# Performance work log

Hardware: AMD Instinct MI355X
Metric: run time of the kernel (lower is better)

## Reference

```python
import jax, jax.numpy as jnp
import numpy as np

EMBED = 256
HEADS = 8
HD = EMBED // HEADS
LEVELS = 4
POINTS = 4
FFN_H = 1024
BS = 8
LQ = 900
SHAPES = [(100, 100), (50, 50), (25, 25), (13, 13)]


def setup_inputs() -> dict:
    key = jax.random.key(0)
    ks = jax.random.split(key, 20)
    nv = sum(h * w for h, w in SHAPES)
    starts = np.cumsum([0] + [h * w for h, w in SHAPES])[:-1]
    inp = {
        "queries": jax.random.normal(ks[0], (BS, LQ, EMBED), jnp.float32),
        "memory": jax.random.normal(ks[1], (BS, nv, EMBED), jnp.float32),
        "query_pos": jax.random.normal(ks[2], (BS, LQ, EMBED), jnp.float32),
        "reference_points": jax.random.uniform(ks[3], (BS, LQ, LEVELS, 4), jnp.float32) * 0.9 + 0.05,
        "spatial_shapes": jnp.asarray(SHAPES, jnp.int32),
        "level_start_index": jnp.asarray(starts, jnp.int32),
    }
    def lin(k, din, dout):
        k1, k2 = jax.random.split(k)
        w = jax.random.normal(k1, (din, dout), jnp.float32) * 0.02
        b = jax.random.normal(k2, (dout,), jnp.float32) * 0.01
        return w, b
    specs = [("Wq", "bq", EMBED, EMBED), ("Wk", "bk", EMBED, EMBED), ("Wv", "bv", EMBED, EMBED),
             ("Wo", "bo", EMBED, EMBED), ("Wvd", "bvd", EMBED, EMBED),
             ("Woff", "boff", EMBED, HEADS * LEVELS * POINTS * 2),
             ("Watt", "batt", EMBED, HEADS * LEVELS * POINTS),
             ("Wop", "bop", EMBED, EMBED), ("Wg", "bg", 2 * EMBED, 2 * EMBED),
             ("W1", "b1", EMBED, FFN_H), ("W2", "b2", FFN_H, EMBED)]
    for i, (wn, bn, di, do) in enumerate(specs):
        w, b = lin(ks[4 + i], di, do)
        inp[wn] = w
        inp[bn] = b
    for n in ["ln1", "ln2", "ln3"]:
        inp[n + "_s"] = jnp.ones((EMBED,), jnp.float32)
        inp[n + "_b"] = jnp.zeros((EMBED,), jnp.float32)
    return inp


def _ln(x, s, b):
    m = jnp.mean(x, -1, keepdims=True)
    v = jnp.mean(jnp.square(x - m), -1, keepdims=True)
    return (x - m) * jax.lax.rsqrt(v + 1e-5) * s + b


def _bilinear(v_l, lx, ly, H, W):
    # v_l: [bs,h,H*W,hd]; lx,ly: [bs,h,lq,p] normalized in [0,1]
    # grid_sample(align_corners=False, padding=zeros) semantics
    px = lx * W - 0.5
    py = ly * H - 0.5
    x0 = jnp.floor(px)
    y0 = jnp.floor(py)
    wx = px - x0
    wy = py - y0
    x0i = x0.astype(jnp.int32)
    y0i = y0.astype(jnp.int32)
    bs, h, lq, p = lx.shape
    out = jnp.zeros((bs, h, lq, p, HD), v_l.dtype)
    for dy in (0, 1):
        for dx in (0, 1):
            xi = x0i + dx
            yi = y0i + dy
            w = (wx if dx else 1.0 - wx) * (wy if dy else 1.0 - wy)
            valid = (xi >= 0) & (xi < W) & (yi >= 0) & (yi < H)
            idx = jnp.clip(yi, 0, H - 1) * W + jnp.clip(xi, 0, W - 1)
            g = jnp.take_along_axis(v_l, idx.reshape(bs, h, lq * p)[..., None], axis=2)
            g = g.reshape(bs, h, lq, p, HD)
            out = out + w[..., None] * jnp.where(valid[..., None], g, 0.0)
    return out


def reference(queries, memory, query_pos, reference_points, spatial_shapes, level_start_index,
              Wq, bq, Wk, bk, Wv, bv, Wo, bo, Wvd, bvd, Woff, boff, Watt, batt, Wop, bop,
              Wg, bg, W1, b1, W2, b2, ln1_s, ln1_b, ln2_s, ln2_b, ln3_s, ln3_b):
    bs, lq, _ = queries.shape
    shp = np.asarray(spatial_shapes)
    st = np.asarray(level_start_index)

    # ---- self attention (pre-norm, q=k=x+pos, v=x) ----
    x = _ln(queries, ln1_s, ln1_b)
    qk = x + query_pos
    Q = (qk @ Wq + bq).reshape(bs, lq, HEADS, HD)
    K = (qk @ Wk + bk).reshape(bs, lq, HEADS, HD)
    V = (x @ Wv + bv).reshape(bs, lq, HEADS, HD)
    scores = jnp.einsum('bqhd,bkhd->bhqk', Q, K) * (1.0 / np.sqrt(HD))
    attn = jax.nn.softmax(scores, axis=-1)
    sa = jnp.einsum('bhqk,bkhd->bqhd', attn, V).reshape(bs, lq, EMBED) @ Wo + bo
    x1 = queries + sa  # dropout is identity in eval

    # ---- MS-deformable cross attention ----
    y = _ln(x1, ln2_s, ln2_b)
    qc = y + query_pos
    val = (memory @ Wvd + bvd).reshape(bs, -1, HEADS, HD).transpose(0, 2, 1, 3)  # [bs,h,Nv,hd]
    off = (qc @ Woff + boff).reshape(bs, lq, HEADS, LEVELS, POINTS, 2)
    aw = jax.nn.softmax((qc @ Watt + batt).reshape(bs, lq, HEADS, LEVELS * POINTS), axis=-1)
    aw = aw.reshape(bs, lq, HEADS, LEVELS, POINTS)
    rp = reference_points[:, :, None, :, None, :]  # [bs,lq,1,L,1,4]
    loc = rp[..., :2] + off / POINTS * rp[..., 2:] * 0.5  # [bs,lq,h,L,p,2]

    out = jnp.zeros((bs, HEADS, lq, HD), queries.dtype)
    for l in range(LEVELS):
        H, W = int(shp[l, 0]), int(shp[l, 1])
        s0 = int(st[l])
        v_l = val[:, :, s0:s0 + H * W]
        lx = jnp.transpose(loc[:, :, :, l, :, 0], (0, 2, 1, 3))  # [bs,h,lq,p]
        ly = jnp.transpose(loc[:, :, :, l, :, 1], (0, 2, 1, 3))
        samp = _bilinear(v_l, lx, ly, H, W)  # [bs,h,lq,p,hd]
        w = jnp.transpose(aw[:, :, :, l], (0, 2, 1, 3))  # [bs,h,lq,p]
        out = out + jnp.sum(w[..., None] * samp, axis=3)
    cross = out.transpose(0, 2, 1, 3).reshape(bs, lq, EMBED) @ Wop + bop

    # ---- gated fusion ----
    gi = jnp.concatenate([x1, cross], axis=-1)
    g = jax.nn.sigmoid(gi @ Wg + bg)
    x2 = g[..., :EMBED] * x1 + g[..., EMBED:] * cross

    # ---- FFN ----
    z = _ln(x2, ln3_s, ln3_b)
    ffn = jax.nn.relu(z @ W1 + b1) @ W2 + b2
    return (x2 + ffn, aw, loc)
```

## Files before the change

kernel.cpp:

```cpp
#include <hip/hip_runtime.h>
#include <hip/hip_bf16.h>
#include <math.h>

#define BB 8
#define LQ 900
#define EE 256
#define NH 8
#define HD 32
#define NL 4
#define NP 4
#define FFN_H 1024

typedef __bf16 bf16x8 __attribute__((ext_vector_type(8)));
typedef float f32x4 __attribute__((ext_vector_type(4)));
typedef unsigned short u16x8 __attribute__((ext_vector_type(8)));

__device__ __forceinline__ unsigned short f2b(float f) {
    union { float f; unsigned int u; } v; v.f = f;
    unsigned int u = v.u;
    unsigned int r = (u + 0x7fffu + ((u >> 16) & 1u)) >> 16;
    return (unsigned short)r;
}
__device__ __forceinline__ float b2f(unsigned short h) {
    union { unsigned int u; float f; } v; v.u = ((unsigned int)h) << 16; return v.f;
}

typedef __attribute__((address_space(3))) unsigned int* lds_ptr_t;
typedef const __attribute__((address_space(1))) unsigned int* gbl_ptr_t;
#define GLOAD16(g, l) __builtin_amdgcn_global_load_lds((gbl_ptr_t)(g), (lds_ptr_t)(l), 16, 0, 0)
#define VMCNT(n) asm volatile("s_waitcnt vmcnt(" #n ")" ::: "memory")

struct TDesc { const float* src; unsigned short* dst; int K, N, tile0; };
struct TPack {
    TDesc d[12];
    const float *bq, *bk, *boff, *batt;
    float *bqk, *boa;
    const float *Wop_src, *Wg_src, *bop_src, *bg_src;
    unsigned short* WopRow;
    float* bgg;
};

__global__ __launch_bounds__(256) void prep_kernel(
    TPack p,
    const float* __restrict__ queries, const float* __restrict__ qpos,
    const float* __restrict__ ln1_s, const float* __restrict__ ln1_b,
    unsigned short* __restrict__ x_b, unsigned short* __restrict__ qk_b)
{
    const int bi = blockIdx.x;
    const int t = threadIdx.x;

    if (bi < 1248) {
        int di = 0;
#pragma unroll
        for (int i = 1; i < 12; ++i) if (bi >= p.d[i].tile0) di = i;
        TDesc d = p.d[di];
        int tt = bi - d.tile0;
        int tn = (d.N + 31) >> 5;
        int tk = tt / tn, tc = tt % tn;
        __shared__ float tile[32][33];
        int tx = t & 31, ty = t >> 5;
#pragma unroll
        for (int i = 0; i < 4; ++i) {
            int kk = tk * 32 + ty + i * 8, nn = tc * 32 + tx;
// ... 35 lines not shown
    }
    {
        const int row = bi - 1286;
        const int w = t >> 6, lane = t & 63;
        __shared__ float red[4];
        float v = queries[(size_t)row * EE + t];
        float sum = v;
#pragma unroll
        for (int o = 32; o; o >>= 1) sum += __shfl_xor(sum, o, 64);
        if (lane == 0) red[w] = sum;
        __syncthreads();
        float mean = (red[0] + red[1] + red[2] + red[3]) * (1.0f / 256.0f);
        __syncthreads();
        float dd = v - mean;
        float sq = dd * dd;
#pragma unroll
        for (int o = 32; o; o >>= 1) sq += __shfl_xor(sq, o, 64);
        if (lane == 0) red[w] = sq;
        __syncthreads();
        float var = (red[0] + red[1] + red[2] + red[3]) * (1.0f / 256.0f);
        float y = dd * rsqrtf(var + 1e-5f) * ln1_s[t] + ln1_b[t];
        x_b[(size_t)row * EE + t]  = f2b(y);
        qk_b[(size_t)row * EE + t] = f2b(y + qpos[(size_t)row * EE + t]);
    }
}

struct GD {
    const unsigned short* A;
    const unsigned short* Bt;
    const float* bias;
    const float* resid;
    float* outF;
    unsigned short* outB;
    const float* lnS; const float* lnB; const float* lnAdd;
    unsigned short* lnOut;
    int M, K, N, ntN, tile0, ldOutB, outBoff, act, ldA;
};
struct GB {
    GD d[3]; int nd, tot;
    const float* castSrc; unsigned short* castDst; long castN;
};

template<int BN>
__global__ __launch_bounds__(256, (BN == 128) ? 4 : 2) void gemm_pipe(GB g) {
    __shared__ __align__(16) unsigned short ldsb[2][(64 + BN) * 32];
    __shared__ float lnred[2][64][2];
    const int tid = threadIdx.x;
    const int l = tid & 63, w = tid >> 6;
    const int wr = w >> 1, wc = w & 1;
    constexpr int NJ = BN / 32;

    int t = blockIdx.x;
    if (t >= g.tot) {
        long i = ((long)(t - g.tot) * 256 + tid) * 8;
        long stride = (long)2048 * 256 * 8;
        for (; i < g.castN; i += stride) {
            float4 a = *(const float4*)(g.castSrc + i);
            float4 b = *(const float4*)(g.castSrc + i + 4);
            u16x8 o;
            o[0] = f2b(a.x); o[1] = f2b(a.y); o[2] = f2b(a.z); o[3] = f2b(a.w);
            o[4] = f2b(b.x); o[5] = f2b(b.y); o[6] = f2b(b.z); o[7] = f2b(b.w);
            *(u16x8*)(g.castDst + i) = o;
        }
        return;
    }
    int d = 0;
    while (d + 1 < g.nd && t >= g.d[d + 1].tile0) ++d;

    auto stage = [&](int dd, int tt, int ks, int pp) {
        const GD& D = g.d[dd];
        const int lda = D.ldA ? D.ldA : D.K;
        int local = tt - D.tile0;
        int m0 = (local / D.ntN) * 64;
        int n0 = (local % D.ntN) * BN;
        unsigned short* base = &ldsb[pp][0];
        {
            int row = w * 16 + (l >> 2);
            int rg = m0 + row; int mm = D.M - 1; rg = rg < mm ? rg : mm;
            int schunk = ((l & 3) ^ ((row >> 1) & 3)) << 4;
            GLOAD16((const char*)(D.A + (size_t)rg * lda + (ks << 5)) + schunk,
                    base + (w * 16) * 32);
        }
#pragma unroll
        for (int ib = 0; ib < BN / 64; ++ib) {
            int row = ib * 64 + w * 16 + (l >> 2);
            int rg = n0 + row; int nn = D.N - 1; rg = rg < nn ? rg : nn;
            int schunk = ((l & 3) ^ ((row >> 1) & 3)) << 4;
            GLOAD16((const char*)(D.Bt + (size_t)rg * D.K + (ks << 5)) + schunk,
                    base + 2048 + (ib * 64 + w * 16) * 32);
        }
    };

    stage(d, t, 0, 0);
    int p = 0;

    while (true) {
        const GD D = g.d[d];
        int local = t - D.tile0;
        const int m0 = (local / D.ntN) * 64;
        const int n0 = (local % D.ntN) * BN;
        const int nk = D.K >> 5;

        f32x4 acc[2][NJ];
#pragma unroll
        for (int i = 0; i < 2; ++i)
#pragma unroll
            for (int j = 0; j < NJ; ++j) acc[i][j] = (f32x4){0.f, 0.f, 0.f, 0.f};

        for (int ks = 0; ks < nk; ++ks) {
            int nt = t, nks = ks + 1, ndd = d;
            bool have = true;
            if (nks == nk) {
                nt = t + gridDim.x; nks = 0;
                if (nt >= g.tot) have = false;
                else { while (ndd + 1 < g.nd && nt >= g.d[ndd + 1].tile0) ++ndd; }
            }
            if (have) {
                stage(ndd, nt, nks, p ^ 1);
                if constexpr (BN == 128) { VMCNT(3); } else { VMCNT(5); }
            } else {
                VMCNT(0);
            }
            __builtin_amdgcn_sched_barrier(0);
            __builtin_amdgcn_s_barrier();
            __builtin_amdgcn_sched_barrier(0);
            {
                const char* base = (const char*)&ldsb[p][0];
                const int rch = ((l >> 4) ^ ((l >> 1) & 3)) << 4;
                bf16x8 af[2];
#pragma unroll
                for (int i = 0; i < 2; ++i) {
                    int row = wr * 32 + i * 16 + (l & 15);
                    af[i] = *(const bf16x8*)(base + row * 64 + rch);
                }
#pragma unroll
                for (int j = 0; j < NJ; ++j) {
                    int row = wc * (BN / 2) + j * 16 + (l & 15);
                    bf16x8 bfr = *(const bf16x8*)(base + 4096 + row * 64 + rch);
#pragma unroll
                    for (int i = 0; i < 2; ++i)
                        acc[i][j] = __builtin_amdgcn_mfma_f32_16x16x32_bf16(af[i], bfr, acc[i][j], 0, 0, 0);
                }
            }
            __builtin_amdgcn_sched_barrier(0);
            __builtin_amdgcn_s_barrier();
            __builtin_amdgcn_sched_barrier(0);
            p ^= 1;
        }

#pragma unroll
        for (int i = 0; i < 2; ++i) {
#pragma unroll
            for (int r = 0; r < 4; ++r) {
                int gm = m0 + wr * 32 + i * 16 + ((l >> 4) << 2) + r;
                if (gm >= D.M) continue;
#pragma unroll
                for (int j = 0; j < NJ; ++j) {
                    int gn = n0 + wc * (BN / 2) + j * 16 + (l & 15);
                    if (gn >= D.N) continue;
                    float v = acc[i][j][r];
                    if (D.bias)  v += D.bias[gn];
                    if (D.resid) v += D.resid[(size_t)gm * D.N + gn];
                    if (D.act == 1)      v = fmaxf(v, 0.f);
                    else if (D.act == 2) v = 1.0f / (1.0f + __expf(-v));
                    acc[i][j][r] = v;
                    if (D.outF) D.outF[(size_t)gm * D.N + gn] = v;
                    if (D.outB) D.outB[(size_t)gm * D.ldOutB + D.outBoff + gn] = f2b(v);
                }
            }
        }

        if constexpr (BN == 256) {
            if (D.lnOut) {
#pragma unroll
                for (int i = 0; i < 2; ++i) {
#pragma unroll
                    for (int r = 0; r < 4; ++r) {
                        float s1 = 0.f, s2 = 0.f;
#pragma unroll
                        for (int j = 0; j < NJ; ++j) {
                            float v = acc[i][j][r];
                            s1 += v; s2 += v * v;
                        }
#pragma unroll
                        for (int o = 1; o <= 8; o <<= 1) {
                            s1 += __shfl_xor(s1, o, 64);
                            s2 += __shfl_xor(s2, o, 64);
                        }
                        if ((l & 15) == 0) {
                            int row = wr * 32 + i * 16 + ((l >> 4) << 2) + r;
                            lnred[wc][row][0] = s1;
                            lnred[wc][row][1] = s2;
                        }
                    }
                }
                __syncthreads();
#pragma unroll
                for (int i = 0; i < 2; ++i) {
#pragma unroll
                    for (int r = 0; r < 4; ++r) {
                        int row = wr * 32 + i * 16 + ((l >> 4) << 2) + r;
                        int gm = m0 + row;
                        if (gm >= D.M) continue;
                        float mean = (lnred[0][row][0] + lnred[1][row][0]) * (1.0f / 256.0f);
                        float msq  = (lnred[0][row][1] + lnred[1][row][1]) * (1.0f / 256.0f);
                        float rs = rsqrtf(msq - mean * mean + 1e-5f);
#pragma unroll
                        for (int j = 0; j < NJ; ++j) {
                            int gn = wc * 128 + j * 16 + (l & 15);
                            float y = (acc[i][j][r] - mean) * rs * D.lnS[gn] + D.lnB[gn]
                                      + D.lnAdd[(size_t)gm * 256 + gn];
                            D.lnOut[(size_t)gm * 256 + gn] = f2b(y);
                        }
                    }
                }
            }
        }

        t += gridDim.x;
        if (t >= g.tot) break;
        while (d + 1 < g.nd && t >= g.d[d + 1].tile0) ++d;
    }
}

#define VGRID 1536

__global__ __launch_bounds__(256) void attn_val(
    const unsigned short* __restrict__ QK, const unsigned short* __restrict__ Vb,
    unsigned short* __restrict__ outB,
    const unsigned short* __restrict__ vA, const unsigned short* __restrict__ vBt,
    const float* __restrict__ vbias, unsigned short* __restrict__ vout,
    int Mv, int vtiles)
{
    __shared__ __align__(16) unsigned short smem[(64 + 128) * 32 * 2];
    const int bid = blockIdx.x;
    const int tid = threadIdx.x;
    const int l = tid & 63, w = tid >> 6;

    if (bid >= 960) {
        const int wr = w >> 1, wc = w & 1;
        int t = bid - 960;
        if (t >= vtiles) return;

        auto stage = [&](int tt, int ks, int pp) {
            unsigned short* base = &smem[pp * 192 * 32];
            int m0 = (tt >> 1) * 64;
            int n0 = (tt & 1) * 128;
            {
                int row = w * 16 + (l >> 2);
                int rg = m0 + row; int mm = Mv - 1; rg = rg < mm ? rg : mm;
                int schunk = ((l & 3) ^ ((row >> 1) & 3)) << 4;
                GLOAD16((const char*)(vA + (size_t)rg * 256 + (ks << 5)) + schunk,
                        base + (w * 16) * 32);
            }
#pragma unroll
            for (int ib = 0; ib < 2; ++ib) {
                int row = ib * 64 + w * 16 + (l >> 2);
                int rg = n0 + row;
                int schunk = ((l & 3) ^ ((row >> 1) & 3)) << 4;
                GLOAD16((const char*)(vBt + (size_t)rg * 256 + (ks << 5)) + schunk,
                        base + 2048 + (ib * 64 + w * 16) * 32);
            }
        };

        stage(t, 0, 0);
        int p = 0;
        while (true) {
            const int m0 = (t >> 1) * 64;
            const int n0 = (t & 1) * 128;

            f32x4 acc[2][4];
#pragma unroll
            for (int i = 0; i < 2; ++i)
#pragma unroll
                for (int j = 0; j < 4; ++j) acc[i][j] = (f32x4){0.f, 0.f, 0.f, 0.f};

            for (int ks = 0; ks < 8; ++ks) {
                int nt = t, nks = ks + 1;
                bool have = true;
                if (nks == 8) {
                    nt = t + VGRID; nks = 0;
                    if (nt >= vtiles) have = false;
                }
                if (have) { stage(nt, nks, p ^ 1); VMCNT(3); }
                else      { VMCNT(0); }
                __builtin_amdgcn_sched_barrier(0);
                __builtin_amdgcn_s_barrier();
                __builtin_amdgcn_sched_barrier(0);
                {
                    const char* base = (const char*)&smem[p * 192 * 32];
                    const int rch = ((l >> 4) ^ ((l >> 1) & 3)) << 4;
                    bf16x8 af[2];
#pragma unroll
                    for (int i = 0; i < 2; ++i) {
                        int row = wr * 32 + i * 16 + (l & 15);
                        af[i] = *(const bf16x8*)(base + row * 64 + rch);
                    }
#pragma unroll
                    for (int j = 0; j < 4; ++j) {
                        int row = wc * 64 + j * 16 + (l & 15);
                        bf16x8 bfr = *(const bf16x8*)(base + 4096 + row * 64 + rch);
#pragma unroll
                        for (int i = 0; i < 2; ++i)
                            acc[i][j] = __builtin_amdgcn_mfma_f32_16x16x32_bf16(af[i], bfr, acc[i][j], 0, 0, 0);
                    }
                }
                __builtin_amdgcn_sched_barrier(0);
                __builtin_amdgcn_s_barrier();
                __builtin_amdgcn_sched_barrier(0);
                p ^= 1;
            }

#pragma unroll
            for (int i = 0; i < 2; ++i) {
#pragma unroll
                for (int r = 0; r < 4; ++r) {
                    int gm = m0 + wr * 32 + i * 16 + ((l >> 4) << 2) + r;
                    if (gm >= Mv) continue;
#pragma unroll
                    for (int j = 0; j < 4; ++j) {
                        int gn = n0 + wc * 64 + j * 16 + (l & 15);
                        float v = acc[i][j][r] + vbias[gn];
                        vout[(size_t)gm * 256 + gn] = f2b(v);
                    }
                }
            }

            t += VGRID;
            if (t >= vtiles) break;
        }
        return;
    }

    const int qt = bid % 15;
    const int bh = bid / 15;
    const int b = bh >> 3, h = bh & 7;

    unsigned short* Ks = smem;
    unsigned short* VT = smem + 2048;
    unsigned short* Ps = smem + 4096;

    const int qrow_w = qt * 64 + w * 16;
// ... 79 lines not shown

#pragma unroll
        for (int s = 0; s < 2; ++s) {
            union { unsigned short u[8]; bf16x8 v; } pb;
#pragma unroll
            for (int j = 0; j < 8; ++j)
                pb.u[j] = pw[(s * 32 + (l >> 4) * 8 + j) * 20 + (l & 15)];
#pragma unroll
            for (int m2 = 0; m2 < 2; ++m2) {
                int dd = m2 * 16 + (l & 15);
                int swz = (((dd & 7) ^ (dd >> 3)) << 4);
                bf16x8 vf = *(const bf16x8*)((const char*)VT + dd * 128 +
                            ((s * 64 + (l >> 4) * 16) ^ swz));
                if (m2 == 0) acc0 = __builtin_amdgcn_mfma_f32_16x16x32_bf16(vf, pb.v, acc0, 0, 0, 0);
                else         acc1 = __builtin_amdgcn_mfma_f32_16x16x32_bf16(vf, pb.v, acc1, 0, 0, 0);
            }
        }
        if (kt < 14) { kvc = kvn; vvc = vvn; }
    }

    float inv = 1.0f / l_run;
    int q = qrow_w + (l & 15);
    if (q < LQ) {
        size_t obase = ((size_t)(b * LQ + q)) * 256 + h * 32;
#pragma unroll
        for (int r = 0; r < 4; ++r) {
            int d0 = (l >> 4) * 4 + r;
            outB[obase + d0]      = f2b(acc0[r] * inv);
            outB[obase + 16 + d0] = f2b(acc1[r] * inv);
        }
    }
}

__global__ __launch_bounds__(256) void sample_fused(
    const float* __restrict__ off_att, const float* __restrict__ refp,
    const unsigned short* __restrict__ val,
    const int* __restrict__ shapes, const int* __restrict__ starts,
    float* __restrict__ aw_out, float* __restrict__ loc_out,
    unsigned short* __restrict__ xs, int NV)
{
    const int row = blockIdx.x;
    const int b = row / LQ;
    const int t = threadIdx.x;
    const int h = t >> 5, d = t & 31;

    __shared__ float l_logit[128];
    __shared__ float l_aw[128];
    __shared__ float l_loc[256];
    __shared__ int l_sh[NL * 2];
    __shared__ int l_st[NL];

    if (t < 128) l_logit[t] = off_att[(size_t)row * 384 + 256 + t];
    {
        float o = off_att[(size_t)row * 384 + t];
        int c = t & 1;
        int lv = (t >> 3) & 3;
        float rc = refp[((size_t)row * 4 + lv) * 4 + c];
        float rs = refp[((size_t)row * 4 + lv) * 4 + 2 + c];
        float loc = rc + o * 0.125f * rs;
        l_loc[t] = loc;
        loc_out[(size_t)row * 256 + t] = loc;
    }
    if (t < NL * 2) l_sh[t] = shapes[t];
    if (t < NL) l_st[t] = starts[t];
    __syncthreads();
    if (t < 128) {
        int hh = t >> 4;
        float mx = -1e30f;
#pragma unroll
        for (int i = 0; i < 16; ++i) mx = fmaxf(mx, l_logit[hh * 16 + i]);
        float sum = 0.f;
#pragma unroll
        for (int i = 0; i < 16; ++i) sum += __expf(l_logit[hh * 16 + i] - mx);
        float aw = __expf(l_logit[t] - mx) / sum;
        l_aw[t] = aw;
        aw_out[(size_t)row * 128 + t] = aw;
    }
    __syncthreads();

    float acc = 0.f;
    const unsigned short* vb = val + (size_t)b * NV * EE + h * HD + d;

#pragma unroll
    for (int lv = 0; lv < NL; ++lv) {
        const int Hh = l_sh[lv * 2], Ww = l_sh[lv * 2 + 1];
        const int s0 = l_st[lv];
#pragma unroll
        for (int p = 0; p < NP; ++p) {
            const int base = ((h * NL + lv) * NP + p) * 2;
            float lx = l_loc[base], ly = l_loc[base + 1];
            float wgt0 = l_aw[h * 16 + lv * NP + p];
            float px = lx * (float)Ww - 0.5f;
            float py = ly * (float)Hh - 0.5f;
            float x0f = floorf(px), y0f = floorf(py);
            float wx = px - x0f, wy = py - y0f;
            int x0 = (int)x0f, y0 = (int)y0f;
#pragma unroll
            for (int dy = 0; dy < 2; ++dy) {
                int yi = y0 + dy;
                bool vy = (yi >= 0) && (yi < Hh);
                int yc = min(max(yi, 0), Hh - 1);
                float wyv = dy ? wy : 1.f - wy;
#pragma unroll
                for (int dx = 0; dx < 2; ++dx) {
                    int xi = x0 + dx;
                    bool vv = vy && (xi >= 0) && (xi < Ww);
                    int xc = min(max(xi, 0), Ww - 1);
                    float wgt = wgt0 * wyv * (dx ? wx : 1.f - wx);
                    float gv = b2f(vb[(size_t)(s0 + yc * Ww + xc) * EE]);
                    acc += vv ? wgt * gv : 0.f;
                }
            }
        }
    }
    xs[(size_t)row * 512 + 256 + t] = f2b(acc);
}

__global__ __launch_bounds__(256) void gate_ln3(
    const float* __restrict__ g, const float* __restrict__ x1,
    const float* __restrict__ cross, const float* __restrict__ s,
    const float* __restrict__ bln, float* __restrict__ x2out,
    unsigned short* __restrict__ zb)
{
    const int row = blockIdx.x;
    const int t = threadIdx.x;
    const int w = t >> 6;
    const int lane = t & 63;
    __shared__ float red[4];

    float g1 = g[(size_t)row * 512 + t];
    float g2 = g[(size_t)row * 512 + 256 + t];
    float v = g1 * x1[(size_t)row * EE + t] + g2 * cross[(size_t)row * EE + t];
    x2out[(size_t)row * EE + t] = v;

    float sum = v;
#pragma unroll
    for (int o = 32; o; o >>= 1) sum += __shfl_xor(sum, o, 64);
    if (lane == 0) red[w] = sum;
    __syncthreads();
    float mean = (red[0] + red[1] + red[2] + red[3]) * (1.0f / 256.0f);
    __syncthreads();

    float d = v - mean;
    float sq = d * d;
#pragma unroll
    for (int o = 32; o; o >>= 1) sq += __shfl_xor(sq, o, 64);
    if (lane == 0) red[w] = sq;
    __syncthreads();
    float var = (red[0] + red[1] + red[2] + red[3]) * (1.0f / 256.0f);

    float y = d * rsqrtf(var + 1e-5f) * s[t] + bln[t];
    zb[(size_t)row * EE + t] = f2b(y);
}

extern "C" void kernel_launch(void* const* d_in, const int* in_sizes, int n_in,
                              void* d_out, int out_size, void* d_ws, size_t ws_size,
                              hipStream_t stream)
{
    const float* queries   = (const float*)d_in[0];
    const float* memory    = (const float*)d_in[1];
    const float* query_pos = (const float*)d_in[2];
    const float* refp      = (const float*)d_in[3];
    const int*   shapes    = (const int*)d_in[4];
    const int*   starts    = (const int*)d_in[5];
    const float* Wq  = (const float*)d_in[6],  *bq  = (const float*)d_in[7];
    const float* Wk  = (const float*)d_in[8],  *bk  = (const float*)d_in[9];
    const float* Wv  = (const float*)d_in[10], *bv  = (const float*)d_in[11];
    const float* Wo  = (const float*)d_in[12], *bo  = (const float*)d_in[13];
    const float* Wvd = (const float*)d_in[14], *bvd = (const float*)d_in[15];
    const float* Woff= (const float*)d_in[16], *boff= (const float*)d_in[17];
    const float* Watt= (const float*)d_in[18], *batt= (const float*)d_in[19];
    const float* Wop = (const float*)d_in[20], *bop = (const float*)d_in[21];
    const float* Wg  = (const float*)d_in[22], *bg  = (const float*)d_in[23];
    const float* W1  = (const float*)d_in[24], *b1  = (const float*)d_in[25];
    const float* W2  = (const float*)d_in[26], *b2  = (const float*)d_in[27];
    const float* ln1_s = (const float*)d_in[28], *ln1_b = (const float*)d_in[29];
    const float* ln2_s = (const float*)d_in[30], *ln2_b = (const float*)d_in[31];
    const float* ln3_s = (const float*)d_in[32], *ln3_b = (const float*)d_in[33];

    const int NV = in_sizes[1] / (BB * EE);
    const int Mq = BB * LQ;
    const int Mv = BB * NV;
    const long memN = (long)Mv * EE;

    char* W8 = (char*)d_ws;
// ... 33 lines not shown
    unsigned short* hidden_b = (unsigned short*)((char*)z_b + (size_t)Mq * 256 * 2);

    float* out0    = (float*)d_out;
    float* aw_out  = out0 + (size_t)Mq * 256;
    float* loc_out = aw_out + (size_t)Mq * 128;

    dim3 blk(256);
    const int tMq = (Mq + 63) / 64;
    const int tv  = (Mv + 63) / 64;

    TPack tp;
    tp.d[0]  = { Wq,             WtQK,             256, 256,    0 };
    tp.d[1]  = { Wk,             WtQK + 256 * 256, 256, 256,   64 };
    tp.d[2]  = { Wv,             WtV,              256, 256,  128 };
    tp.d[3]  = { Wo,             WtO,              256, 256,  192 };
    tp.d[4]  = { Wvd,            WtVD,             256, 256,  256 };
    tp.d[5]  = { Woff,           WtOA,             256, 256,  320 };
    tp.d[6]  = { Watt,           WtOA + 256 * 256, 256, 128,  384 };
    tp.d[7]  = { Wop,            WtOP,             256, 256,  416 };
    tp.d[8]  = { Wg,             WtGF,             512, 512,  480 };
    tp.d[9]  = { Wg + 256 * 512, Wg2T,             256, 512,  608 };
    tp.d[10] = { W1,             Wt1,              256, 1024, 736 };
    tp.d[11] = { W2,             Wt2,             1024, 256,  992 };
    tp.bq = bq; tp.bk = bk; tp.boff = boff; tp.batt = batt;
    tp.bqk = bqk; tp.boa = boa;
    tp.Wop_src = Wop; tp.Wg_src = Wg; tp.bop_src = bop; tp.bg_src = bg;
    tp.WopRow = WopRow; tp.bgg = bgg;
    prep_kernel<<<8486, blk, 0, stream>>>(
        tp, queries, query_pos, ln1_s, ln1_b, x_b, qk_b);

    {
        GB g; g.nd = 3;
        g.d[0] = { qk_b, WtQK, bqk, nullptr, nullptr, qkb,
                   nullptr, nullptr, nullptr, nullptr,
                   Mq, 256, 512, 4, 0, 512, 0, 0, 0 };
        g.d[1] = { x_b, WtV, bv, nullptr, nullptr, vb_buf,
                   nullptr, nullptr, nullptr, nullptr,
                   Mq, 256, 256, 2, tMq * 4, 256, 0, 0, 0 };
        g.d[2] = { Wg2T, WopRow, nullptr, nullptr, nullptr, WtGF,
                   nullptr, nullptr, nullptr, nullptr,
                   512, 256, 256, 2, tMq * 6, 512, 256, 0, 0 };
        g.tot = tMq * 6 + 16;
        g.castSrc = memory; g.castDst = mem_b; g.castN = memN;
        gemm_pipe<128><<<g.tot + 2048, blk, 0, stream>>>(g);
    }

    attn_val<<<960 + VGRID, blk, 0, stream>>>(
        qkb, vb_buf, av_buf, mem_b, WtVD, bvd, val_b, Mv, tv * 2);

    {
        GB g; g.nd = 1;
        g.d[0] = { av_buf, WtO, bo, queries, x1, xs_cat,
                   ln2_s, ln2_b, query_pos, qc_b,
                   Mq, 256, 256, 1, 0, 512, 0, 0, 0 };
        g.tot = tMq;
        g.castSrc = nullptr; g.castDst = nullptr; g.castN = 0;
        gemm_pipe<256><<<tMq, blk, 0, stream>>>(g);
    }

    {
        GB g; g.nd = 1;
        g.d[0] = { qc_b, WtOA, boa, nullptr, off_att, nullptr,
                   nullptr, nullptr, nullptr, nullptr,
                   Mq, 256, 384, 3, 0, 384, 0, 0, 0 };
        g.tot = tMq * 3;
        g.castSrc = nullptr; g.castDst = nullptr; g.castN = 0;
        gemm_pipe<128><<<g.tot, blk, 0, stream>>>(g);
    }

    sample_fused<<<Mq, blk, 0, stream>>>(off_att, refp, val_b, shapes, starts,
                                         aw_out, loc_out, xs_cat, NV);

    {
        GB g; g.nd = 2;
        g.d[0] = { xs_cat + 256, WtOP, bop, nullptr, cross, nullptr,
                   nullptr, nullptr, nullptr, nullptr,
                   Mq, 256, 256, 2, 0, 0, 0, 0, 512 };
        g.d[1] = { xs_cat, WtGF, bgg, nullptr, gbuf, nullptr,
                   nullptr, nullptr, nullptr, nullptr,
                   Mq, 512, 512, 4, tMq * 2, 0, 0, 2, 0 };
        g.tot = tMq * 6;
        g.castSrc = nullptr; g.castDst = nullptr; g.castN = 0;
        gemm_pipe<128><<<g.tot, blk, 0, stream>>>(g);
    }

    gate_ln3<<<Mq, blk, 0, stream>>>(gbuf, x1, cross, ln3_s, ln3_b, x2, z_b);

    {
        GB g; g.nd = 1;
        g.d[0] = { z_b, Wt1, b1, nullptr, nullptr, hidden_b,
                   nullptr, nullptr, nullptr, nullptr,
                   Mq, 256, 1024, 8, 0, 1024, 0, 1, 0 };
        g.tot = tMq * 8;
        g.castSrc = nullptr; g.castDst = nullptr; g.castN = 0;
        gemm_pipe<128><<<g.tot, blk, 0, stream>>>(g);
    }

    {
        GB g; g.nd = 1;
        g.d[0] = { hidden_b, Wt2, b2, x2, out0, nullptr,
                   nullptr, nullptr, nullptr, nullptr,
                   Mq, 1024, 256, 2, 0, 256, 0, 0, 0 };
        g.tot = tMq * 2;
        g.castSrc = nullptr; g.castDst = nullptr; g.castN = 0;
        gemm_pipe<128><<<g.tot, blk, 0, stream>>>(g);
    }
}
```

Baseline: 305.6 us.

## Merge post-attention stages into one cooperative persistent megakernel with grid syncs

Replaces the separate launches after attn_val (output projection, LN2, offset/attention GEMM, sampling, cross/gate GEMMs, gate+LN3, FFN GEMMs) with a single cooperative kernel that runs each stage as a grid-stride loop and separates stages with grid-wide syncs. It also drops the BN=256 GEMM variant with its fused LN epilogue, computing LN2 as a separate row pass inside the megakernel. The aim is to remove launch overhead and inter-kernel gaps. In exchange, each stage loses its own tuned grid and occupancy, tile GEMMs no longer prefetch across tiles, and grid.sync adds its own cost.

After: 657.8 us. 2.15x slower.

```diff
diff --git a/kernel.cpp b/kernel.cpp
--- a/kernel.cpp
+++ b/kernel.cpp
@@ -1,6 +1,9 @@
 #include <hip/hip_runtime.h>
 #include <hip/hip_bf16.h>
+#include <hip/hip_cooperative_groups.h>
 #include <math.h>
+
+namespace cg = cooperative_groups;
 
 #define BB 8
 #define LQ 900
@@ -29,6 +32,7 @@
 typedef const __attribute__((address_space(1))) unsigned int* gbl_ptr_t;
 #define GLOAD16(g, l) __builtin_amdgcn_global_load_lds((gbl_ptr_t)(g), (lds_ptr_t)(l), 16, 0, 0)
 #define VMCNT(n) asm volatile("s_waitcnt vmcnt(" #n ")" ::: "memory")
+#define SBAR() do { __builtin_amdgcn_sched_barrier(0); __builtin_amdgcn_s_barrier(); __builtin_amdgcn_sched_barrier(0); } while (0)
 
 struct TDesc { const float* src; unsigned short* dst; int K, N, tile0; };
 struct TPack {
@@ -130,8 +134,6 @@
     const float* resid;
     float* outF;
     unsigned short* outB;
-    const float* lnS; const float* lnB; const float* lnAdd;
-    unsigned short* lnOut;
     int M, K, N, ntN, tile0, ldOutB, outBoff, act, ldA;
 };
 struct GB {
@@ -139,14 +141,11 @@
     const float* castSrc; unsigned short* castDst; long castN;
 };
 
-template<int BN>
-__global__ __launch_bounds__(256, (BN == 128) ? 4 : 2) void gemm_pipe(GB g) {
-    __shared__ __align__(16) unsigned short ldsb[2][(64 + BN) * 32];
-    __shared__ float lnred[2][64][2];
+__global__ __launch_bounds__(256, 4) void gemm_pipe(GB g) {
+    __shared__ __align__(16) unsigned short ldsb[2][192 * 32];
     const int tid = threadIdx.x;
     const int l = tid & 63, w = tid >> 6;
     const int wr = w >> 1, wc = w & 1;
-    constexpr int NJ = BN / 32;
 
     int t = blockIdx.x;
     if (t >= g.tot) {
@@ -170,21 +169,21 @@
         const int lda = D.ldA ? D.ldA : D.K;
         int local = tt - D.tile0;
         int m0 = (local / D.ntN) * 64;
-        int n0 = (local % D.ntN) * BN;
+        int n0 = (local % D.ntN) * 128;
         unsigned short* base = &ldsb[pp][0];
         {
             int row = w * 16 + (l >> 2);
             int rg = m0 + row; int mm = D.M - 1; rg = rg < mm ? rg : mm;
-            int schunk = ((l & 3) ^ ((row >> 1) & 3)) << 4;
-            GLOAD16((const char*)(D.A + (size_t)rg * lda + (ks << 5)) + schunk,
+            int sch = ((l & 3) ^ ((row >> 1) & 3)) << 4;
+            GLOAD16((const char*)(D.A + (size_t)rg * lda + (ks << 5)) + sch,
                     base + (w * 16) * 32);
         }
 #pragma unroll
-        for (int ib = 0; ib < BN / 64; ++ib) {
+        for (int ib = 0; ib < 2; ++ib) {
             int row = ib * 64 + w * 16 + (l >> 2);
             int rg = n0 + row; int nn = D.N - 1; rg = rg < nn ? rg : nn;
-            int schunk = ((l & 3) ^ ((row >> 1) & 3)) << 4;
-            GLOAD16((const char*)(D.Bt + (size_t)rg * D.K + (ks << 5)) + schunk,
+            int sch = ((l & 3) ^ ((row >> 1) & 3)) << 4;
+            GLOAD16((const char*)(D.Bt + (size_t)rg * D.K + (ks << 5)) + sch,
                     base + 2048 + (ib * 64 + w * 16) * 32);
         }
     };
@@ -196,14 +195,14 @@
         const GD D = g.d[d];
         int local = t - D.tile0;
         const int m0 = (local / D.ntN) * 64;
-        const int n0 = (local % D.ntN) * BN;
+        const int n0 = (local % D.ntN) * 128;
         const int nk = D.K >> 5;
 
-        f32x4 acc[2][NJ];
+        f32x4 acc[2][4];
 #pragma unroll
         for (int i = 0; i < 2; ++i)
 #pragma unroll
-            for (int j = 0; j < NJ; ++j) acc[i][j] = (f32x4){0.f, 0.f, 0.f, 0.f};
+            for (int j = 0; j < 4; ++j) acc[i][j] = (f32x4){0.f, 0.f, 0.f, 0.f};
 
         for (int ks = 0; ks < nk; ++ks) {
             int nt = t, nks = ks + 1, ndd = d;
@@ -213,15 +212,9 @@
                 if (nt >= g.tot) have = false;
                 else { while (ndd + 1 < g.nd && nt >= g.d[ndd + 1].tile0) ++ndd; }
             }
-            if (have) {
-                stage(ndd, nt, nks, p ^ 1);
-                if constexpr (BN == 128) { VMCNT(3); } else { VMCNT(5); }
-            } else {
-                VMCNT(0);
-            }
-            __builtin_amdgcn_sched_barrier(0);
-            __builtin_amdgcn_s_barrier();
-            __builtin_amdgcn_sched_barrier(0);
+            if (have) { stage(ndd, nt, nks, p ^ 1); VMCNT(3); }
+            else      { VMCNT(0); }
+            SBAR();
             {
                 const char* base = (const char*)&ldsb[p][0];
                 const int rch = ((l >> 4) ^ ((l >> 1) & 3)) << 4;
@@ -232,17 +225,15 @@
                     af[i] = *(const bf16x8*)(base + row * 64 + rch);
                 }
 #pragma unroll
-                for (int j = 0; j < NJ; ++j) {
-                    int row = wc * (BN / 2) + j * 16 + (l & 15);
+                for (int j = 0; j < 4; ++j) {
+                    int row = wc * 64 + j * 16 + (l & 15);
                     bf16x8 bfr = *(const bf16x8*)(base + 4096 + row * 64 + rch);
 #pragma unroll
                     for (int i = 0; i < 2; ++i)
                         acc[i][j] = __builtin_amdgcn_mfma_f32_16x16x32_bf16(af[i], bfr, acc[i][j], 0, 0, 0);
                 }
             }
-            __builtin_amdgcn_sched_barrier(0);
-            __builtin_amdgcn_s_barrier();
-            __builtin_amdgcn_sched_barrier(0);
+            SBAR();
             p ^= 1;
         }
 
@@ -253,64 +244,16 @@
                 int gm = m0 + wr * 32 + i * 16 + ((l >> 4) << 2) + r;
                 if (gm >= D.M) continue;
 #pragma unroll
-                for (int j = 0; j < NJ; ++j) {
-                    int gn = n0 + wc * (BN / 2) + j * 16 + (l & 15);
+                for (int j = 0; j < 4; ++j) {
+                    int gn = n0 + wc * 64 + j * 16 + (l & 15);
                     if (gn >= D.N) continue;
                     float v = acc[i][j][r];
                     if (D.bias)  v += D.bias[gn];
                     if (D.resid) v += D.resid[(size_t)gm * D.N + gn];
                     if (D.act == 1)      v = fmaxf(v, 0.f);
                     else if (D.act == 2) v = 1.0f / (1.0f + __expf(-v));
-                    acc[i][j][r] = v;
                     if (D.outF) D.outF[(size_t)gm * D.N + gn] = v;
                     if (D.outB) D.outB[(size_t)gm * D.ldOutB + D.outBoff + gn] = f2b(v);
-                }
-            }
-        }
-
-        if constexpr (BN == 256) {
-            if (D.lnOut) {
-#pragma unroll
-                for (int i = 0; i < 2; ++i) {
-#pragma unroll
-                    for (int r = 0; r < 4; ++r) {
-                        float s1 = 0.f, s2 = 0.f;
-#pragma unroll
-                        for (int j = 0; j < NJ; ++j) {
-                            float v = acc[i][j][r];
-                            s1 += v; s2 += v * v;
-                        }
-#pragma unroll
-                        for (int o = 1; o <= 8; o <<= 1) {
-                            s1 += __shfl_xor(s1, o, 64);
-                            s2 += __shfl_xor(s2, o, 64);
-                        }
-                        if ((l & 15) == 0) {
-                            int row = wr * 32 + i * 16 + ((l >> 4) << 2) + r;
-                            lnred[wc][row][0] = s1;
-                            lnred[wc][row][1] = s2;
-                        }
-                    }
-                }
-                __syncthreads();
-#pragma unroll
-                for (int i = 0; i < 2; ++i) {
-#pragma unroll
-                    for (int r = 0; r < 4; ++r) {
-                        int row = wr * 32 + i * 16 + ((l >> 4) << 2) + r;
-                        int gm = m0 + row;
-                        if (gm >= D.M) continue;
-                        float mean = (lnred[0][row][0] + lnred[1][row][0]) * (1.0f / 256.0f);
-                        float msq  = (lnred[0][row][1] + lnred[1][row][1]) * (1.0f / 256.0f);
-                        float rs = rsqrtf(msq - mean * mean + 1e-5f);
-#pragma unroll
-                        for (int j = 0; j < NJ; ++j) {
-                            int gn = wc * 128 + j * 16 + (l & 15);
-                            float y = (acc[i][j][r] - mean) * rs * D.lnS[gn] + D.lnB[gn]
-                                      + D.lnAdd[(size_t)gm * 256 + gn];
-                            D.lnOut[(size_t)gm * 256 + gn] = f2b(y);
-                        }
-                    }
                 }
             }
         }
@@ -330,7 +273,7 @@
     const float* __restrict__ vbias, unsigned short* __restrict__ vout,
     int Mv, int vtiles)
 {
-    __shared__ __align__(16) unsigned short smem[(64 + 128) * 32 * 2];
+    __shared__ __align__(16) unsigned short smem[192 * 32 * 2];
     const int bid = blockIdx.x;
     const int tid = threadIdx.x;
     const int l = tid & 63, w = tid >> 6;
@@ -347,16 +290,16 @@
             {
                 int row = w * 16 + (l >> 2);
                 int rg = m0 + row; int mm = Mv - 1; rg = rg < mm ? rg : mm;
-                int schunk = ((l & 3) ^ ((row >> 1) & 3)) << 4;
-                GLOAD16((const char*)(vA + (size_t)rg * 256 + (ks << 5)) + schunk,
+                int sch = ((l & 3) ^ ((row >> 1) & 3)) << 4;
+                GLOAD16((const char*)(vA + (size_t)rg * 256 + (ks << 5)) + sch,
                         base + (w * 16) * 32);
             }
 #pragma unroll
             for (int ib = 0; ib < 2; ++ib) {
                 int row = ib * 64 + w * 16 + (l >> 2);
                 int rg = n0 + row;
-                int schunk = ((l & 3) ^ ((row >> 1) & 3)) << 4;
-                GLOAD16((const char*)(vBt + (size_t)rg * 256 + (ks << 5)) + schunk,
+                int sch = ((l & 3) ^ ((row >> 1) & 3)) << 4;
+                GLOAD16((const char*)(vBt + (size_t)rg * 256 + (ks << 5)) + sch,
                         base + 2048 + (ib * 64 + w * 16) * 32);
             }
         };
@@ -382,9 +325,7 @@
                 }
                 if (have) { stage(nt, nks, p ^ 1); VMCNT(3); }
                 else      { VMCNT(0); }
-                __builtin_amdgcn_sched_barrier(0);
-                __builtin_amdgcn_s_barrier();
-                __builtin_amdgcn_sched_barrier(0);
+                SBAR();
                 {
                     const char* base = (const char*)&smem[p * 192 * 32];
                     const int rch = ((l >> 4) ^ ((l >> 1) & 3)) << 4;
@@ -403,9 +344,7 @@
                             acc[i][j] = __builtin_amdgcn_mfma_f32_16x16x32_bf16(af[i], bfr, acc[i][j], 0, 0, 0);
                     }
                 }
-                __builtin_amdgcn_sched_barrier(0);
-                __builtin_amdgcn_s_barrier();
-                __builtin_amdgcn_sched_barrier(0);
+                SBAR();
                 p ^= 1;
             }
 
@@ -551,125 +490,275 @@
     }
 }
 
-__global__ __launch_bounds__(256) void sample_fused(
-    const float* __restrict__ off_att, const float* __restrict__ refp,
-    const unsigned short* __restrict__ val,
-    const int* __restrict__ shapes, const int* __restrict__ starts,
-    float* __restrict__ aw_out, float* __restrict__ loc_out,
-    unsigned short* __restrict__ xs, int NV)
+struct MegaArgs {
+    const unsigned short *av_buf, *WtO;
+    const float *bo, *queries, *qpos, *ln2_s, *ln2_b;
+    float* x1;
+    unsigned short *xs_cat, *qc_b;
+    const unsigned short* WtOA;
+    const float* boa;
+    float* off_att;
+    const float* refp;
+    const unsigned short* val_b;
+    const int *shapes, *starts;
+    float *aw_out, *loc_out;
+    const unsigned short *WtOP, *WtGF;
+    const float *bop, *bgg;
+    float *crossF, *gbuf;
+    const float *ln3_s, *ln3_b;
+    float* x2;
+    unsigned short* z_b;
+    const unsigned short *Wt1, *Wt2;
+    const float *b1, *b2;
+    unsigned short* hidden_b;
+    float* out0;
+    int NV;
+};
+
+__device__ __forceinline__ void tile_gemm(
+    unsigned short* arena,
+    const unsigned short* A, int lda, const unsigned short* Bt,
+    const float* bias, const float* resid,
+    float* outF, unsigned short* outB, int ldOutB, int outBoff,
+    int M, int K, int N, int ntN, int act,
+    int tiles, int bid, int G, int tid)
 {
-    const int row = blockIdx.x;
-    const int b = row / LQ;
-    const int t = threadIdx.x;
-    const int h = t >> 5, d = t & 31;
-
-    __shared__ float l_logit[128];
-    __shared__ float l_aw[128];
-    __shared__ float l_loc[256];
-    __shared__ int l_sh[NL * 2];
-    __shared__ int l_st[NL];
-
-    if (t < 128) l_logit[t] = off_att[(size_t)row * 384 + 256 + t];
+    const int l = tid & 63, w = tid >> 6;
+    const int wr = w >> 1, wc = w & 1;
+    const int nk = K >> 5;
+    for (int t = bid; t < tiles; t += G) {
+        const int m0 = (t / ntN) * 64;
+        const int n0 = (t % ntN) * 128;
+        auto stage = [&](int ks, int pp) {
+            unsigned short* base = arena + pp * 192 * 32;
+            {
+                int row = w * 16 + (l >> 2);
+                int rg = m0 + row; int mm = M - 1; rg = rg < mm ? rg : mm;
+                int sch = ((l & 3) ^ ((row >> 1) & 3)) << 4;
+                GLOAD16((const char*)(A + (size_t)rg * lda + (ks << 5)) + sch,
+                        base + (w * 16) * 32);
+            }
+#pragma unroll
+            for (int ib = 0; ib < 2; ++ib) {
+                int row = ib * 64 + w * 16 + (l >> 2);
+                int rg = n0 + row; int nn = N - 1; rg = rg < nn ? rg : nn;
+                int sch = ((l & 3) ^ ((row >> 1) & 3)) << 4;
+                GLOAD16((const char*)(Bt + (size_t)rg * K + (ks << 5)) + sch,
+                        base + 2048 + (ib * 64 + w * 16) * 32);
+            }
+        };
+        f32x4 acc[2][4];
+#pragma unroll
+        for (int i = 0; i < 2; ++i)
+#pragma unroll
+            for (int j = 0; j < 4; ++j) acc[i][j] = (f32x4){0.f, 0.f, 0.f, 0.f};
+
+        stage(0, 0);
+        int p = 0;
+        for (int ks = 0; ks < nk; ++ks) {
+            if (ks + 1 < nk) { stage(ks + 1, p ^ 1); VMCNT(3); }
+            else             { VMCNT(0); }
+            SBAR();
+            {
+                const char* base = (const char*)(arena + p * 192 * 32);
+                const int rch = ((l >> 4) ^ ((l >> 1) & 3)) << 4;
+                bf16x8 af[2];
+#pragma unroll
+                for (int i = 0; i < 2; ++i) {
+                    int row = wr * 32 + i * 16 + (l & 15);
+                    af[i] = *(const bf16x8*)(base + row * 64 + rch);
+                }
+#pragma unroll
+                for (int j = 0; j < 4; ++j) {
+                    int row = wc * 64 + j * 16 + (l & 15);
+                    bf16x8 bfr = *(const bf16x8*)(base + 4096 + row * 64 + rch);
+#pragma unroll
+                    for (int i = 0; i < 2; ++i)
+                        acc[i][j] = __builtin_amdgcn_mfma_f32_16x16x32_bf16(af[i], bfr, acc[i][j], 0, 0, 0);
+                }
+            }
+            SBAR();
+            p ^= 1;
+        }
+
+#pragma unroll
+        for (int i = 0; i < 2; ++i) {
+#pragma unroll
+            for (int r = 0; r < 4; ++r) {
+                int gm = m0 + wr * 32 + i * 16 + ((l >> 4) << 2) + r;
+                if (gm >= M) continue;
+#pragma unroll
+                for (int j = 0; j < 4; ++j) {
+                    int gn = n0 + wc * 64 + j * 16 + (l & 15);
+                    if (gn >= N) continue;
+                    float v = acc[i][j][r];
+                    if (bias)  v += bias[gn];
+                    if (resid) v += resid[(size_t)gm * N + gn];
+                    if (act == 1)      v = fmaxf(v, 0.f);
+                    else if (act == 2) v = 1.0f / (1.0f + __expf(-v));
+                    if (outF) outF[(size_t)gm * N + gn] = v;
+                    if (outB) outB[(size_t)gm * ldOutB + outBoff + gn] = f2b(v);
+                }
+            }
+        }
+        __syncthreads();
+    }
+}
+
+__global__ __launch_bounds__(256) void mega_kernel(MegaArgs a) {
+    cg::grid_group gg = cg::this_grid();
+    __shared__ __align__(16) unsigned short arena[192 * 32 * 2];
+    const int tid = threadIdx.x;
+    const int bid = blockIdx.x;
+    const int G = gridDim.x;
+    const int w = tid >> 6, lane = tid & 63;
+    float* red = (float*)arena;
+
+    tile_gemm(arena, a.av_buf, 256, a.WtO, a.bo, a.queries, a.x1, a.xs_cat,
+              512, 0, 7200, 256, 256, 2, 0, 226, bid, G, tid);
+    gg.sync();
+
+    for (int row = bid; row < 7200; row += G) {
+        float v = a.x1[(size_t)row * 256 + tid];
+        float sum = v;
+#pragma unroll
+        for (int o = 32; o; o >>= 1) sum += __shfl_xor(sum, o, 64);
+        if (lane == 0) red[w] = sum;
+        __syncthreads();
+        float mean = (red[0] + red[1] + red[2] + red[3]) * (1.0f / 256.0f);
+        __syncthreads();
+        float dd = v - mean;
+        float sq = dd * dd;
+#pragma unroll
+        for (int o = 32; o; o >>= 1) sq += __shfl_xor(sq, o, 64);
+        if (lane == 0) red[w] = sq;
+        __syncthreads();
+        float var = (red[0] + red[1] + red[2] + red[3]) * (1.0f / 256.0f);
+        float y = dd * rsqrtf(var + 1e-5f) * a.ln2_s[tid] + a.ln2_b[tid]
+                  + a.qpos[(size_t)row * 256 + tid];
+        a.qc_b[(size_t)row * 256 + tid] = f2b(y);
+        __syncthreads();
+    }
+    gg.sync();
+
+    tile_gemm(arena, a.qc_b, 256, a.WtOA, a.boa, nullptr, a.off_att, nullptr,
+              0, 0, 7200, 256, 384, 3, 0, 339, bid, G, tid);
+    gg.sync();
+
     {
-        float o = off_att[(size_t)row * 384 + t];
-        int c = t & 1;
-        int lv = (t >> 3) & 3;
-        float rc = refp[((size_t)row * 4 + lv) * 4 + c];
-        float rs = refp[((size_t)row * 4 + lv) * 4 + 2 + c];
-        float loc = rc + o * 0.125f * rs;
-        l_loc[t] = loc;
-        loc_out[(size_t)row * 256 + t] = loc;
-    }
-    if (t < NL * 2) l_sh[t] = shapes[t];
-    if (t < NL) l_st[t] = starts[t];
-    __syncthreads();
-    if (t < 128) {
-        int hh = t >> 4;
-        float mx = -1e30f;
-#pragma unroll
-        for (int i = 0; i < 16; ++i) mx = fmaxf(mx, l_logit[hh * 16 + i]);
-        float sum = 0.f;
-#pragma unroll
-        for (int i = 0; i < 16; ++i) sum += __expf(l_logit[hh * 16 + i] - mx);
-        float aw = __expf(l_logit[t] - mx) / sum;
-        l_aw[t] = aw;
-        aw_out[(size_t)row * 128 + t] = aw;
-    }
-    __syncthreads();
-
-    float acc = 0.f;
-    const unsigned short* vb = val + (size_t)b * NV * EE + h * HD + d;
-
-#pragma unroll
-    for (int lv = 0; lv < NL; ++lv) {
-        const int Hh = l_sh[lv * 2], Ww = l_sh[lv * 2 + 1];
-        const int s0 = l_st[lv];
-#pragma unroll
-        for (int p = 0; p < NP; ++p) {
-            const int base = ((h * NL + lv) * NP + p) * 2;
-            float lx = l_loc[base], ly = l_loc[base + 1];
-            float wgt0 = l_aw[h * 16 + lv * NP + p];
-            float px = lx * (float)Ww - 0.5f;
-            float py = ly * (float)Hh - 0.5f;
-            float x0f = floorf(px), y0f = floorf(py);
-            float wx = px - x0f, wy = py - y0f;
-            int x0 = (int)x0f, y0 = (int)y0f;
-#pragma unroll
-            for (int dy = 0; dy < 2; ++dy) {
-                int yi = y0 + dy;
-                bool vy = (yi >= 0) && (yi < Hh);
-                int yc = min(max(yi, 0), Hh - 1);
-                float wyv = dy ? wy : 1.f - wy;
-#pragma unroll
-                for (int dx = 0; dx < 2; ++dx) {
-                    int xi = x0 + dx;
-                    bool vv = vy && (xi >= 0) && (xi < Ww);
-                    int xc = min(max(xi, 0), Ww - 1);
-                    float wgt = wgt0 * wyv * (dx ? wx : 1.f - wx);
-                    float gv = b2f(vb[(size_t)(s0 + yc * Ww + xc) * EE]);
-                    acc += vv ? wgt * gv : 0.f;
-                }
-            }
-        }
-    }
-    xs[(size_t)row * 512 + 256 + t] = f2b(acc);
-}
-
-__global__ __launch_bounds__(256) void gate_ln3(
-    const float* __restrict__ g, const float* __restrict__ x1,
-    const float* __restrict__ cross, const float* __restrict__ s,
-    const float* __restrict__ bln, float* __restrict__ x2out,
-    unsigned short* __restrict__ zb)
-{
-    const int row = blockIdx.x;
-    const int t = threadIdx.x;
-    const int w = t >> 6;
-    const int lane = t & 63;
-    __shared__ float red[4];
-
-    float g1 = g[(size_t)row * 512 + t];
-    float g2 = g[(size_t)row * 512 + 256 + t];
-    float v = g1 * x1[(size_t)row * EE + t] + g2 * cross[(size_t)row * EE + t];
-    x2out[(size_t)row * EE + t] = v;
-
-    float sum = v;
-#pragma unroll
-    for (int o = 32; o; o >>= 1) sum += __shfl_xor(sum, o, 64);
-    if (lane == 0) red[w] = sum;
-    __syncthreads();
-    float mean = (red[0] + red[1] + red[2] + red[3]) * (1.0f / 256.0f);
-    __syncthreads();
-
-    float d = v - mean;
-    float sq = d * d;
-#pragma unroll
-    for (int o = 32; o; o >>= 1) sq += __shfl_xor(sq, o, 64);
-    if (lane == 0) red[w] = sq;
-    __syncthreads();
-    float var = (red[0] + red[1] + red[2] + red[3]) * (1.0f / 256.0f);
-
-    float y = d * rsqrtf(var + 1e-5f) * s[t] + bln[t];
-    zb[(size_t)row * EE + t] = f2b(y);
+        float* l_logit = (float*)arena;
+        float* l_aw    = l_logit + 128;
+        float* l_loc   = l_aw + 128;
+        int*   l_sh    = (int*)(l_loc + 256);
+        int*   l_st    = l_sh + 8;
+        const int h = tid >> 5, d = tid & 31;
+        for (int row = bid; row < 7200; row += G) {
+            const int b = row / LQ;
+            if (tid < 128) l_logit[tid] = a.off_att[(size_t)row * 384 + 256 + tid];
+            {
+                float o = a.off_att[(size_t)row * 384 + tid];
+                int c = tid & 1;
+                int lv = (tid >> 3) & 3;
+                float rc = a.refp[((size_t)row * 4 + lv) * 4 + c];
+                float rs = a.refp[((size_t)row * 4 + lv) * 4 + 2 + c];
+                float loc = rc + o * 0.125f * rs;
+                l_loc[tid] = loc;
+                a.loc_out[(size_t)row * 256 + tid] = loc;
+            }
+            if (tid < NL * 2) l_sh[tid] = a.shapes[tid];
+            if (tid < NL) l_st[tid] = a.starts[tid];
+            __syncthreads();
+            if (tid < 128) {
+                int hh = tid >> 4;
+                float mx = -1e30f;
+#pragma unroll
+                for (int i = 0; i < 16; ++i) mx = fmaxf(mx, l_logit[hh * 16 + i]);
+                float sum = 0.f;
+#pragma unroll
+                for (int i = 0; i < 16; ++i) sum += __expf(l_logit[hh * 16 + i] - mx);
+                float aw = __expf(l_logit[tid] - mx) / sum;
+                l_aw[tid] = aw;
+                a.aw_out[(size_t)row * 128 + tid] = aw;
+            }
+            __syncthreads();
+
+            float acc = 0.f;
+            const unsigned short* vb = a.val_b + (size_t)b * a.NV * EE + h * HD + d;
+#pragma unroll
+            for (int lv = 0; lv < NL; ++lv) {
+                const int Hh = l_sh[lv * 2], Ww = l_sh[lv * 2 + 1];
+                const int s0 = l_st[lv];
+#pragma unroll
+                for (int p = 0; p < NP; ++p) {
+                    const int base = ((h * NL + lv) * NP + p) * 2;
+                    float lx = l_loc[base], ly = l_loc[base + 1];
+                    float wgt0 = l_aw[h * 16 + lv * NP + p];
+                    float px = lx * (float)Ww - 0.5f;
+                    float py = ly * (float)Hh - 0.5f;
+                    float x0f = floorf(px), y0f = floorf(py);
+                    float wx = px - x0f, wy = py - y0f;
+                    int x0 = (int)x0f, y0 = (int)y0f;
+#pragma unroll
+                    for (int dy = 0; dy < 2; ++dy) {
+                        int yi = y0 + dy;
+                        bool vy = (yi >= 0) && (yi < Hh);
+                        int yc = min(max(yi, 0), Hh - 1);
+                        float wyv = dy ? wy : 1.f - wy;
+#pragma unroll
+                        for (int dx = 0; dx < 2; ++dx) {
+                            int xi = x0 + dx;
+                            bool vv = vy && (xi >= 0) && (xi < Ww);
+                            int xc = min(max(xi, 0), Ww - 1);
+                            float wgt = wgt0 * wyv * (dx ? wx : 1.f - wx);
+                            float gv = b2f(vb[(size_t)(s0 + yc * Ww + xc) * EE]);
+                            acc += vv ? wgt * gv : 0.f;
+                        }
+                    }
+                }
+            }
+            a.xs_cat[(size_t)row * 512 + 256 + tid] = f2b(acc);
+            __syncthreads();
+        }
+    }
+    gg.sync();
+
+    tile_gemm(arena, a.xs_cat + 256, 512, a.WtOP, a.bop, nullptr, a.crossF, nullptr,
+              0, 0, 7200, 256, 256, 2, 0, 226, bid, G, tid);
+    tile_gemm(arena, a.xs_cat, 512, a.WtGF, a.bgg, nullptr, a.gbuf, nullptr,
+              0, 0, 7200, 512, 512, 4, 2, 452, bid, G, tid);
+    gg.sync();
+
+    for (int row = bid; row < 7200; row += G) {
+        float g1 = a.gbuf[(size_t)row * 512 + tid];
+        float g2 = a.gbuf[(size_t)row * 512 + 256 + tid];
+        float v = g1 * a.x1[(size_t)row * 256 + tid] + g2 * a.crossF[(size_t)row * 256 + tid];
+        a.x2[(size_t)row * 256 + tid] = v;
+        float sum = v;
+#pragma unroll
+        for (int o = 32; o; o >>= 1) sum += __shfl_xor(sum, o, 64);
+        if (lane == 0) red[w] = sum;
+        __syncthreads();
+        float mean = (red[0] + red[1] + red[2] + red[3]) * (1.0f / 256.0f);
+        __syncthreads();
+        float dd = v - mean;
+        float sq = dd * dd;
+#pragma unroll
+        for (int o = 32; o; o >>= 1) sq += __shfl_xor(sq, o, 64);
+        if (lane == 0) red[w] = sq;
+        __syncthreads();
+        float var = (red[0] + red[1] + red[2] + red[3]) * (1.0f / 256.0f);
+        float y = dd * rsqrtf(var + 1e-5f) * a.ln3_s[tid] + a.ln3_b[tid];
+        a.z_b[(size_t)row * 256 + tid] = f2b(y);
+        __syncthreads();
+    }
+    gg.sync();
+
+    tile_gemm(arena, a.z_b, 256, a.Wt1, a.b1, nullptr, nullptr, a.hidden_b,
+              1024, 0, 7200, 256, 1024, 8, 1, 904, bid, G, tid);
+    gg.sync();
+
+    tile_gemm(arena, a.hidden_b, 1024, a.Wt2, a.b2, a.x2, a.out0, nullptr,
+              0, 0, 7200, 1024, 256, 2, 0, 226, bid, G, tid);
 }
 
 extern "C" void kernel_launch(void* const* d_in, const int* in_sizes, int n_in,
@@ -769,77 +858,40 @@
     {
         GB g; g.nd = 3;
         g.d[0] = { qk_b, WtQK, bqk, nullptr, nullptr, qkb,
-                   nullptr, nullptr, nullptr, nullptr,
                    Mq, 256, 512, 4, 0, 512, 0, 0, 0 };
         g.d[1] = { x_b, WtV, bv, nullptr, nullptr, vb_buf,
-                   nullptr, nullptr, nullptr, nullptr,
                    Mq, 256, 256, 2, tMq * 4, 256, 0, 0, 0 };
         g.d[2] = { Wg2T, WopRow, nullptr, nullptr, nullptr, WtGF,
-                   nullptr, nullptr, nullptr, nullptr,
                    512, 256, 256, 2, tMq * 6, 512, 256, 0, 0 };
         g.tot = tMq * 6 + 16;
         g.castSrc = memory; g.castDst = mem_b; g.castN = memN;
-        gemm_pipe<128><<<g.tot + 2048, blk, 0, stream>>>(g);
+        gemm_pipe<<<g.tot + 2048, blk, 0, stream>>>(g);
     }
 
     attn_val<<<960 + VGRID, blk, 0, stream>>>(
         qkb, vb_buf, av_buf, mem_b, WtVD, bvd, val_b, Mv, tv * 2);
 
     {
-        GB g; g.nd = 1;
-        g.d[0] = { av_buf, WtO, bo, queries, x1, xs_cat,
-                   ln2_s, ln2_b, query_pos, qc_b,
-                   Mq, 256, 256, 1, 0, 512, 0, 0, 0 };
-        g.tot = tMq;
-        g.castSrc = nullptr; g.castDst = nullptr; g.castN = 0;
-        gemm_pipe<256><<<tMq, blk, 0, stream>>>(g);
-    }
-
-    {
-        GB g; g.nd = 1;
-        g.d[0] = { qc_b, WtOA, boa, nullptr, off_att, nullptr,
-                   nullptr, nullptr, nullptr, nullptr,
-                   Mq, 256, 384, 3, 0, 384, 0, 0, 0 };
-        g.tot = tMq * 3;
-        g.castSrc = nullptr; g.castDst = nullptr; g.castN = 0;
-        gemm_pipe<128><<<g.tot, blk, 0, stream>>>(g);
-    }
-
-    sample_fused<<<Mq, blk, 0, stream>>>(off_att, refp, val_b, shapes, starts,
-                                         aw_out, loc_out, xs_cat, NV);
-
-    {
-        GB g; g.nd = 2;
-        g.d[0] = { xs_cat + 256, WtOP, bop, nullptr, cross, nullptr,
-                   nullptr, nullptr, nullptr, nullptr,
-                   Mq, 256, 256, 2, 0, 0, 0, 0, 512 };
-        g.d[1] = { xs_cat, WtGF, bgg, nullptr, gbuf, nullptr,
-                   nullptr, nullptr, nullptr, nullptr,
-                   Mq, 512, 512, 4, tMq * 2, 0, 0, 2, 0 };
-        g.tot = tMq * 6;
-        g.castSrc = nullptr; g.castDst = nullptr; g.castN = 0;
-        gemm_pipe<128><<<g.tot, blk, 0, stream>>>(g);
-    }
-
-    gate_ln3<<<Mq, blk, 0, stream>>>(gbuf, x1, cross, ln3_s, ln3_b, x2, z_b);
-
-    {
-        GB g; g.nd = 1;
-        g.d[0] = { z_b, Wt1, b1, nullptr, nullptr, hidden_b,
-                   nullptr, nullptr, nullptr, nullptr,
-                   Mq, 256, 1024, 8, 0, 1024, 0, 1, 0 };
-        g.tot = tMq * 8;
-        g.castSrc = nullptr; g.castDst = nullptr; g.castN = 0;
-        gemm_pipe<128><<<g.tot, blk, 0, stream>>>(g);
-    }
-
-    {
-        GB g; g.nd = 1;
-        g.d[0] = { hidden_b, Wt2, b2, x2, out0, nullptr,
-                   nullptr, nullptr, nullptr, nullptr,
-                   Mq, 1024, 256, 2, 0, 256, 0, 0, 0 };
-        g.tot = tMq * 2;
-        g.castSrc = nullptr; g.castDst = nullptr; g.castN = 0;
-        gemm_pipe<128><<<g.tot, blk, 0, stream>>>(g);
+        MegaArgs ma;
+        ma.av_buf = av_buf; ma.WtO = WtO; ma.bo = bo; ma.queries = queries;
+        ma.qpos = query_pos; ma.ln2_s = ln2_s; ma.ln2_b = ln2_b;
+        ma.x1 = x1; ma.xs_cat = xs_cat; ma.qc_b = qc_b;
+        ma.WtOA = WtOA; ma.boa = boa; ma.off_att = off_att;
+        ma.refp = refp; ma.val_b = val_b; ma.shapes = shapes; ma.starts = starts;
+        ma.aw_out = aw_out; ma.loc_out = loc_out;
+        ma.WtOP = WtOP; ma.WtGF = WtGF; ma.bop = bop; ma.bgg = bgg;
+        ma.crossF = cross; ma.gbuf = gbuf;
+        ma.ln3_s = ln3_s; ma.ln3_b = ln3_b; ma.x2 = x2; ma.z_b = z_b;
+        ma.Wt1 = Wt1; ma.Wt2 = Wt2; ma.b1 = b1; ma.b2 = b2;
+        ma.hidden_b = hidden_b; ma.out0 = out0;
+        ma.NV = NV;
+
+        int nb = 0;
+        hipOccupancyMaxActiveBlocksPerMultiprocessor(&nb, (const void*)mega_kernel, 256, 0);
+        if (nb < 1) nb = 1;
+        int G = nb * 256;
+        if (G > 1536) G = 1536;
+        void* kp[] = { (void*)&ma };
+        hipLaunchCooperativeKernel((const void*)mega_kernel, dim3(G), blk, kp, 0, stream);
     }
 }
```
